# Performance work log

Hardware: AMD Instinct MI355X
Metric: run time of the kernel (lower is better)

## Reference

```python
import jax, jax.numpy as jnp
import numpy as np

N_NODES = 100000


def _segment_mean(h, src, dst, n_nodes):
    # copy_u: gather source features along edges, then mean-reduce per dst node
    msg = h[src]                                             # [E, D]
    s = jax.ops.segment_sum(msg, dst, num_segments=n_nodes)  # [N, D]
    cnt = jax.ops.segment_sum(jnp.ones((src.shape[0],), h.dtype), dst,
                              num_segments=n_nodes)          # [N]
    return s / jnp.maximum(cnt, 1.0)[:, None]


def setup_inputs() -> dict:
    key = jax.random.key(0)
    k1, k2, k3, k4, k5 = jax.random.split(key, 5)
    in_feats, n_hidden, n_classes = 128, 128, 64
    n_edges = 1600000
    features = jax.random.normal(k1, (N_NODES, in_feats), dtype=jnp.float32)
    W1 = jax.random.normal(k2, (in_feats, n_hidden), dtype=jnp.float32) * (1.0 / np.sqrt(in_feats))
    b1 = jnp.zeros((n_hidden,), jnp.float32)
    W2 = jax.random.normal(k3, (n_hidden, n_classes), dtype=jnp.float32) * (1.0 / np.sqrt(n_hidden))
    b2 = jnp.zeros((n_classes,), jnp.float32)
    src = jax.random.randint(k4, (n_edges,), 0, N_NODES, dtype=jnp.int64)
    dst = jax.random.randint(k5, (n_edges,), 0, N_NODES, dtype=jnp.int64)
    return {"features": features, "W1": W1, "b1": b1, "W2": W2, "b2": b2,
            "src": src, "dst": dst}


def reference(features, W1, b1, W2, b2, src, dst):
    # Layer 0: mean aggregation -> Linear -> relu  (dropout p=0.0 is identity)
    h = _segment_mean(features, src, dst, N_NODES)
    h = jax.nn.relu(h @ W1 + b1)
    # Layer 1: mean aggregation -> Linear (no activation on output layer)
    h = _segment_mean(h, src, dst, N_NODES)
    h = h @ W2 + b2
    return h
```

## Files before the change

kernel.cpp:

```cpp
#include <hip/hip_runtime.h>

#define N_NODES 100000
#define D 128
#define NE 1600000
#define C_OUT 64
#define NB 391
#define SENT 100000
#define P2B 256
#define P2E 6250
#define SEGSTRIDE 6400

typedef _Float16 half8 __attribute__((ext_vector_type(8)));
typedef float floatx4 __attribute__((ext_vector_type(4)));


__device__ inline half8 shfl_xor_h8(half8 v, int mask) {
    union { half8 h; int i[4]; } u;
    u.h = v;
    u.i[0] = __shfl_xor(u.i[0], mask);
    u.i[1] = __shfl_xor(u.i[1], mask);
    u.i[2] = __shfl_xor(u.i[2], mask);
    u.i[3] = __shfl_xor(u.i[3], mask);
    return u.h;
}

__device__ inline void pack_one(const float* W, _Float16* Wp, int tid, int N) {
    int l = tid & 63, p = tid >> 6;
    int nt = p >> 2, kc = p & 3;
    int quad = l >> 4, c = l & 15;
    int n = nt * 16 + c;
    half8 h;
    #pragma unroll
    for (int j = 0; j < 8; ++j) {
        int k = kc * 32 + quad * 8 + j;
        h[j] = (_Float16)W[k * N + n];
    }
    *(half8*)(Wp + (size_t)p * 512 + l * 8) = h;
}

__global__ __launch_bounds__(256) void setup_kernel(const float* __restrict__ W1,
                                                    const float* __restrict__ W2,
                                                    _Float16* __restrict__ wp1,
                                                    _Float16* __restrict__ wp2,
                                                    int* __restrict__ t1s,
                                                    int* __restrict__ t2s) {
    const int blk = blockIdx.x;
    const int t = threadIdx.x;
    if (blk < 8) {
        pack_one(W1, wp1, blk * 256 + t, 128);
    } else if (blk < 12) {
        pack_one(W2, wp2, (blk - 8) * 256 + t, 64);
    } else {
        if (t < 64) t1s[t] = 0;
        else if (t < 96) t2s[t - 64] = 0;
    }
}

__global__ __launch_bounds__(1024) void p2_part(const int* __restrict__ src,
                                                const int* __restrict__ dst,
                                                unsigned* __restrict__ gwords,
                                                int* __restrict__ ofsg) {
    __shared__ unsigned ebuf[P2E];
    __shared__ int hist[NB];
    __shared__ int ofs[NB + 1];
    __shared__ int cur[NB];
    __shared__ int wsum[8];
    const int t = threadIdx.x;
    const int base = blockIdx.x * P2E;

    for (int i = t; i < NB; i += 1024) hist[i] = 0;
    __syncthreads();

    unsigned w[7];
    int bk[7];
    #pragma unroll
    for (int r = 0; r < 7; ++r) {
        const int j = r * 1024 + t;
        if (j < P2E) {
            const int e = base + j;
            const int d = dst[e];
            w[r] = ((unsigned)(d & 255) << 20) | (unsigned)src[e];
            bk[r] = d >> 8;
            atomicAdd(&hist[bk[r]], 1);
        } else {
            bk[r] = -1;
        }
    }
    __syncthreads();

    int v = 0, incl = 0;
    if (t < 512) { v = (t < NB) ? hist[t] : 0; incl = v; }
    #pragma unroll
    for (int d = 1; d < 64; d <<= 1) {
        int y = __shfl_up(incl, d);
        if ((t & 63) >= d) incl += y;
    }
    if (t < 512 && (t & 63) == 63) wsum[t >> 6] = incl;
    __syncthreads();
    if (t < NB) {
        int ex = incl - v;
        const int wv = t >> 6;
        for (int j = 0; j < wv; ++j) ex += wsum[j];
        ofs[t] = ex;
        cur[t] = ex;
    }
    if (t == 0) ofs[NB] = P2E;
    __syncthreads();

    #pragma unroll
    for (int r = 0; r < 7; ++r) {
        if (bk[r] >= 0) {
            const int slot = atomicAdd(&cur[bk[r]], 1);
            ebuf[slot] = w[r];
        }
    }
    __syncthreads();

    unsigned* gout = gwords + (size_t)blockIdx.x * SEGSTRIDE;
    for (int i = t; i < P2E; i += 1024) gout[i] = ebuf[i];
    int* oout = ofsg + blockIdx.x * (NB + 1);
    for (int i = t; i < NB + 1; i += 1024) oout[i] = ofs[i];
}

__global__ __launch_bounds__(256) void p_sum(const int* __restrict__ ofsg,
                                             int* __restrict__ btot) {
    __shared__ int ws4[4];
    const int b = blockIdx.x;
    const int t = threadIdx.x;
    const int* row = ofsg + t * (NB + 1);
    int d = row[b + 1] - row[b];
    #pragma unroll
    for (int m = 1; m < 64; m <<= 1) d += __shfl_xor(d, m);
    if ((t & 63) == 0) ws4[t >> 6] = d;
    __syncthreads();
    if (t == 0) btot[b] = ws4[0] + ws4[1] + ws4[2] + ws4[3];
}

__global__ __launch_bounds__(512) void p_scanB(const int* __restrict__ btot,
                                               int* __restrict__ bbase) {
    __shared__ int wsum[8];
    const int t = threadIdx.x;
    int v = (t < NB) ? btot[t] : 0;
    int incl = v;
    #pragma unroll
    for (int d = 1; d < 64; d <<= 1) {
        int y = __shfl_up(incl, d);
        if ((t & 63) >= d) incl += y;
    }
    if ((t & 63) == 63) wsum[t >> 6] = incl;
    __syncthreads();
    int ex = incl - v;
    const int wv = t >> 6;
    for (int j = 0; j < wv; ++j) ex += wsum[j];
    if (t < NB) bbase[t] = ex;
    if (t == 0) bbase[NB] = NE;
}

__global__ __launch_bounds__(256) void p3_finalize(const unsigned* __restrict__ gwords,
                                                   const int* __restrict__ ofsg,
                                                   const int* __restrict__ bbase,
                                                   int* __restrict__ ptrp,
                                                   int* __restrict__ pcnt,
                                                   float* __restrict__ inv,
                                                   int* __restrict__ csr) {
    __shared__ unsigned wbuf[8192];
    __shared__ int lcnt[256];
    __shared__ int lofs[256];
    __shared__ int ws4[4];
    __shared__ int cursor;
    const int b = blockIdx.x;
    const int t = threadIdx.x;
    if (t == 0) cursor = 0;
    lcnt[t] = 0;
    __syncthreads();

    for (int blk = t; blk < P2B; blk += 256) {
        const int* row = ofsg + blk * (NB + 1);
        const int a = row[b];
        const int len = row[b + 1] - a;
        if (len > 0) {
            const int o = atomicAdd(&cursor, len);
            if (o + len <= 8192) {
                const unsigned* s = gwords + (size_t)blk * SEGSTRIDE + a;
                for (int j = 0; j < len; ++j) {
                    const unsigned w = s[j];
                    wbuf[o + j] = w;
                    atomicAdd(&lcnt[(w >> 20) & 255], 1);
                }
            }
        }
    }
    __syncthreads();

    const int tot = cursor;
    const int v = lcnt[t];
    const int pc = (v + 7) & ~7;
    int incl = pc;
    #pragma unroll
    for (int d = 1; d < 64; d <<= 1) {
        int y = __shfl_up(incl, d);
        if ((t & 63) >= d) incl += y;
    }
    if ((t & 63) == 63) ws4[t >> 6] = incl;
    __syncthreads();
    int ex = incl - pc;
    {
        const int wv = t >> 6;
        for (int j = 0; j < wv; ++j) ex += ws4[j];
    }
    const int pad_base = bbase[b] + 1792 * b;

    const int node = b * 256 + t;
    if (node < N_NODES) {
        ptrp[node] = pad_base + ex;
        pcnt[node] = pc;
        inv[node] = 1.0f / fmaxf((float)v, 1.0f);
    }
    for (int j = v; j < pc; ++j) csr[pad_base + ex + j] = SENT;

    __syncthreads();
    lofs[t] = ex;
    __syncthreads();
    for (int i = t; i < tot; i += 256) {
        const unsigned w = wbuf[i];
        const int pos = atomicAdd(&lofs[(w >> 20) & 255], 1);
        csr[pad_base + pos] = (int)(w & 0xFFFFF);
    }
}

__global__ __launch_bounds__(256) void gemm1(const float* __restrict__ A,
                                             const _Float16* __restrict__ Wp,
                                             _Float16* __restrict__ outh) {
    __shared__ __align__(16) _Float16 Wl[16384];
    __shared__ __align__(16) _Float16 Al[4096];
    const int t = threadIdx.x;
    {
        const floatx4* s4 = (const floatx4*)Wp;
        floatx4* d4 = (floatx4*)Wl;
        #pragma unroll
        for (int i = 0; i < 8; ++i) d4[t + 256 * i] = s4[t + 256 * i];
    }
    const int lane = t & 63;
    const int wave = t >> 6;
    const int row0 = blockIdx.x * 128;

    floatx4 acc[8][2];
    #pragma unroll
    for (int mt = 0; mt < 8; ++mt)
        #pragma unroll
        for (int nt = 0; nt < 2; ++nt) acc[mt][nt] = (floatx4)0.0f;

    for (int kc = 0; kc < 4; ++kc) {
        __syncthreads();
        #pragma unroll
        for (int rep = 0; rep < 2; ++rep) {
            int p = rep * 256 + t;
            int r = p >> 2, quad = p & 3;
            int row = row0 + r;
            if (row > N_NODES - 1) row = N_NODES - 1;
            const float4 x0 = *(const float4*)(A + (size_t)row * D + kc * 32 + quad * 8);
            const float4 x1 = *(const float4*)(A + (size_t)row * D + kc * 32 + quad * 8 + 4);
            half8 h;
            h[0] = (_Float16)x0.x; h[1] = (_Float16)x0.y;
            h[2] = (_Float16)x0.z; h[3] = (_Float16)x0.w;
            h[4] = (_Float16)x1.x; h[5] = (_Float16)x1.y;
            h[6] = (_Float16)x1.z; h[7] = (_Float16)x1.w;
            int mt = r >> 4, m = r & 15;
            *(half8*)(Al + mt * 512 + (quad * 16 + m) * 8) = h;
        }
        __syncthreads();
        const half8* Af = (const half8*)Al;
        const half8* Bf = (const half8*)Wl;
        half8 b0 = Bf[((wave * 2 + 0) * 4 + kc) * 64 + lane];
        half8 b1 = Bf[((wave * 2 + 1) * 4 + kc) * 64 + lane];
        #pragma unroll
        for (int mt = 0; mt < 8; ++mt) {
            half8 a = Af[mt * 64 + lane];
            acc[mt][0] = __builtin_amdgcn_mfma_f32_16x16x32_f16(a, b0, acc[mt][0], 0, 0, 0);
            acc[mt][1] = __builtin_amdgcn_mfma_f32_16x16x32_f16(a, b1, acc[mt][1], 0, 0, 0);
        }
    }

    const int quad = lane >> 4, cl = lane & 15;
    #pragma unroll
    for (int mt = 0; mt < 8; ++mt)
        #pragma unroll
        for (int nt = 0; nt < 2; ++nt) {
            int col = wave * 32 + nt * 16 + cl;
            #pragma unroll
            for (int i = 0; i < 4; ++i) {
                int row = row0 + mt * 16 + quad * 4 + i;
                if (row < N_NODES)
                    outh[(size_t)row * D + col] = (_Float16)acc[mt][nt][i];
            }
        }
}

__global__ __launch_bounds__(256) void gemm2(const _Float16* __restrict__ Ah,
                                             const _Float16* __restrict__ Wp,
                                             _Float16* __restrict__ outh) {
    __shared__ __align__(16) _Float16 Wl[8192];
    __shared__ __align__(16) _Float16 Al[4096];
    const int t = threadIdx.x;
    {
        const floatx4* s4 = (const floatx4*)Wp;
        floatx4* d4 = (floatx4*)Wl;
        #pragma unroll
        for (int i = 0; i < 4; ++i) d4[t + 256 * i] = s4[t + 256 * i];
    }
    const int lane = t & 63;
    const int wave = t >> 6;
    const int row0 = blockIdx.x * 128;

    floatx4 acc[8];
    #pragma unroll
    for (int mt = 0; mt < 8; ++mt) acc[mt] = (floatx4)0.0f;

    for (int kc = 0; kc < 4; ++kc) {
        __syncthreads();
        #pragma unroll
        for (int rep = 0; rep < 2; ++rep) {
            int p = rep * 256 + t;
            int r = p >> 2, quad = p & 3;
            int row = row0 + r;
            if (row > N_NODES - 1) row = N_NODES - 1;
            half8 h = *(const half8*)(Ah + (size_t)row * D + kc * 32 + quad * 8);
            int mt = r >> 4, m = r & 15;
            *(half8*)(Al + mt * 512 + (quad * 16 + m) * 8) = h;
        }
        __syncthreads();
        const half8* Af = (const half8*)Al;
        const half8* Bf = (const half8*)Wl;
        half8 b = Bf[(wave * 4 + kc) * 64 + lane];
        #pragma unroll
        for (int mt = 0; mt < 8; ++mt) {
            half8 a = Af[mt * 64 + lane];
            acc[mt] = __builtin_amdgcn_mfma_f32_16x16x32_f16(a, b, acc[mt], 0, 0, 0);
        }
    }

    const int quad = lane >> 4, cl = lane & 15;
    const int col = wave * 16 + cl;
    #pragma unroll
    for (int mt = 0; mt < 8; ++mt)
        #pragma unroll
        for (int i = 0; i < 4; ++i) {
            int row = row0 + mt * 16 + quad * 4 + i;
            if (row < N_NODES)
                outh[(size_t)row * C_OUT + col] = (_Float16)acc[mt][i];
        }
}

__global__ __launch_bounds__(256) void agg128h(const _Float16* __restrict__ f,
                                               const int* __restrict__ ptrp,
                                               const int* __restrict__ pcnt,
                                               const int* __restrict__ csr,
                                               const float* __restrict__ inv,
                                               const float* __restrict__ bias,
                                               _Float16* __restrict__ outh) {
    const int wave = threadIdx.x >> 6;
    const int lane = threadIdx.x & 63;
    const int q = lane & 15, hf = lane >> 4;
    const int n = blockIdx.x * 4 + wave;
    const int begin = ptrp[n];
    const int end = begin + pcnt[n];
    const float iv = inv[n];
    const half8* f8 = (const half8*)f;

    half8 acc0 = {0, 0, 0, 0, 0, 0, 0, 0};
    half8 acc1 = {0, 0, 0, 0, 0, 0, 0, 0};
    for (int base = begin; base < end; base += 64) {
        const int m = min(64, end - base);
        int edge = (lane < m) ? csr[base + lane] : SENT;
        int i = 0;
        for (; i + 16 <= m; i += 16) {
            int s0 = __shfl(edge, i + hf);
            int s1 = __shfl(edge, i + 4 + hf);
            int s2 = __shfl(edge, i + 8 + hf);
            int s3 = __shfl(edge, i + 12 + hf);
            half8 v0 = f8[(size_t)s0 * 16 + q];
            half8 v1 = f8[(size_t)s1 * 16 + q];
            half8 v2 = f8[(size_t)s2 * 16 + q];
            half8 v3 = f8[(size_t)s3 * 16 + q];
            acc0 += v0;
            acc1 += v1;
            acc0 += v2;
            acc1 += v3;
        }
        if (i < m) {
            int s0 = __shfl(edge, i + hf);
            int s1 = __shfl(edge, i + 4 + hf);
            half8 v0 = f8[(size_t)s0 * 16 + q];
            half8 v1 = f8[(size_t)s1 * 16 + q];
            acc0 += v0;
            acc1 += v1;
        }
    }
    acc0 += acc1;
    acc0 += shfl_xor_h8(acc0, 16);
    acc0 += shfl_xor_h8(acc0, 32);
    if (hf == 0) {
        const float4 b0 = ((const float4*)bias)[q * 2];
        const float4 b1 = ((const float4*)bias)[q * 2 + 1];
        half8 o;
        o[0] = (_Float16)fmaxf((float)acc0[0] * iv + b0.x, 0.f);
        o[1] = (_Float16)fmaxf((float)acc0[1] * iv + b0.y, 0.f);
        o[2] = (_Float16)fmaxf((float)acc0[2] * iv + b0.z, 0.f);
        o[3] = (_Float16)fmaxf((float)acc0[3] * iv + b0.w, 0.f);
        o[4] = (_Float16)fmaxf((float)acc0[4] * iv + b1.x, 0.f);
        o[5] = (_Float16)fmaxf((float)acc0[5] * iv + b1.y, 0.f);
        o[6] = (_Float16)fmaxf((float)acc0[6] * iv + b1.z, 0.f);
        o[7] = (_Float16)fmaxf((float)acc0[7] * iv + b1.w, 0.f);
        ((half8*)outh)[(size_t)n * 16 + q] = o;
    }
}

__global__ __launch_bounds__(256) void agg64h(const _Float16* __restrict__ f,
                                              const int* __restrict__ ptrp,
                                              const int* __restrict__ pcnt,
                                              const int* __restrict__ csr,
                                              const float* __restrict__ inv,
                                              const float* __restrict__ bias,
                                              float* __restrict__ out) {
    const int wave = threadIdx.x >> 6;
    const int lane = threadIdx.x & 63;
    const int q = lane & 7, hf = lane >> 3;
    const int n = blockIdx.x * 4 + wave;
    const int begin = ptrp[n];
    const int end = begin + pcnt[n];
    const float iv = inv[n];
    const half8* f8 = (const half8*)f;

    half8 acc0 = {0, 0, 0, 0, 0, 0, 0, 0};
    half8 acc1 = {0, 0, 0, 0, 0, 0, 0, 0};
    for (int base = begin; base < end; base += 64) {
        const int m = min(64, end - base);
        int edge = (lane < m) ? csr[base + lane] : SENT;
        int i = 0;
        for (; i + 32 <= m; i += 32) {
            int s0 = __shfl(edge, i + hf);
            int s1 = __shfl(edge, i + 8 + hf);
            int s2 = __shfl(edge, i + 16 + hf);
            int s3 = __shfl(edge, i + 24 + hf);
            half8 v0 = f8[(size_t)s0 * 8 + q];
            half8 v1 = f8[(size_t)s1 * 8 + q];
            half8 v2 = f8[(size_t)s2 * 8 + q];
            half8 v3 = f8[(size_t)s3 * 8 + q];
            acc0 += v0;
            acc1 += v1;
            acc0 += v2;
            acc1 += v3;
        }
        if (i + 16 <= m) {
            int s0 = __shfl(edge, i + hf);
            int s1 = __shfl(edge, i + 8 + hf);
            half8 v0 = f8[(size_t)s0 * 8 + q];
            half8 v1 = f8[(size_t)s1 * 8 + q];
            acc0 += v0;
            acc1 += v1;
            i += 16;
        }
        if (i < m) {
            int s = __shfl(edge, i + hf);
            acc0 += f8[(size_t)s * 8 + q];
        }
    }
    acc0 += acc1;
    acc0 += shfl_xor_h8(acc0, 8);
    acc0 += shfl_xor_h8(acc0, 16);
    acc0 += shfl_xor_h8(acc0, 32);
    if (hf == 0) {
        const float4 b0 = ((const float4*)bias)[q * 2];
        const float4 b1 = ((const float4*)bias)[q * 2 + 1];
        float4 o0, o1;
        o0.x = (float)acc0[0] * iv + b0.x;
        o0.y = (float)acc0[1] * iv + b0.y;
        o0.z = (float)acc0[2] * iv + b0.z;
        o0.w = (float)acc0[3] * iv + b0.w;
        o1.x = (float)acc0[4] * iv + b1.x;
        o1.y = (float)acc0[5] * iv + b1.y;
        o1.z = (float)acc0[6] * iv + b1.z;
        o1.w = (float)acc0[7] * iv + b1.w;
        ((float4*)out)[(size_t)n * 16 + q * 2] = o0;
        ((float4*)out)[(size_t)n * 16 + q * 2 + 1] = o1;
    }
}

extern "C" void kernel_launch(void* const* d_in, const int* in_sizes, int n_in,
                              void* d_out, int out_size, void* d_ws, size_t ws_size,
                              hipStream_t stream) {
    const float* features = (const float*)d_in[0];
    const float* W1 = (const float*)d_in[1];
    const float* b1 = (const float*)d_in[2];
    const float* W2 = (const float*)d_in[3];
    const float* b2 = (const float*)d_in[4];
    const int* src = (const int*)d_in[5];
    const int* dst = (const int*)d_in[6];
    float* out = (float*)d_out;

    char* ws = (char*)d_ws;
    int*      bbase = (int*)(ws + 0L * 4);
    int*      ofsg  = (int*)(ws + 512L * 4);
    int*      btot  = (int*)(ws + 100864L * 4);
    int*      ptrp  = (int*)(ws + 125952L * 4);
    int*      pcnt  = (int*)(ws + 225952L * 4);
    float*    inv   = (float*)(ws + 325952L * 4);
    int*      csr   = (int*)(ws + 425952L * 4);
    unsigned* gwords= (unsigned*)(ws + 2825952L * 4);
    _Float16* wp1   = (_Float16*)(ws + 4464352L * 4);
    _Float16* wp2   = (_Float16*)(ws + 4472544L * 4);
    _Float16* t1h   = (_Float16*)(ws + 4476640L * 4);
    _Float16* h1h   = (_Float16*)(ws + 10876704L * 4);
    _Float16* t2h   = (_Float16*)(ws + 17276704L * 4);

    setup_kernel<<<13, 256, 0, stream>>>(W1, W2, wp1, wp2,
                                         (int*)(t1h + (size_t)SENT * 128),
                                         (int*)(t2h + (size_t)SENT * 64));
    p2_part<<<P2B, 1024, 0, stream>>>(src, dst, gwords, ofsg);
    p_sum<<<NB, 256, 0, stream>>>(ofsg, btot);
    p_scanB<<<1, 512, 0, stream>>>(btot, bbase);
    p3_finalize<<<NB, 256, 0, stream>>>(gwords, ofsg, bbase, ptrp, pcnt, inv, csr);

    const int gemm_grid = (N_NODES + 127) / 128;

    gemm1<<<gemm_grid, 256, 0, stream>>>(features, wp1, t1h);
    agg128h<<<N_NODES / 4, 256, 0, stream>>>(t1h, ptrp, pcnt, csr, inv, b1, h1h);

    gemm2<<<gemm_grid, 256, 0, stream>>>(h1h, wp2, t2h);
    agg64h<<<N_NODES / 4, 256, 0, stream>>>(t2h, ptrp, pcnt, csr, inv, b2, out);
}
```

Before: 250.2 us.

## Fuse pipeline stages into fewer kernel launches and merge aggregation with GEMM2

Merges the weight-packing setup into the partition kernel, and the per-bucket sum into the first GEMM launch as extra blocks. The separate bucket scan is removed: each finalize block recomputes its own prefix from btot. Layer-1 aggregation is fused with the second GEMM so the aggregated hidden features stay in LDS and never go to global memory. This cuts launch count and the global round-trip of the h1 buffer. The cost is redundant prefix sums per block and heterogeneous blocks with larger shared memory that may lower occupancy.

```diff
diff --git a/kernel.cpp b/kernel.cpp
--- a/kernel.cpp
+++ b/kernel.cpp
@@ -38,28 +38,32 @@
     *(half8*)(Wp + (size_t)p * 512 + l * 8) = h;
 }
 
-__global__ __launch_bounds__(256) void setup_kernel(const float* __restrict__ W1,
+__global__ __launch_bounds__(1024) void k1_p2_setup(const int* __restrict__ src,
+                                                    const int* __restrict__ dst,
+                                                    unsigned* __restrict__ gwords,
+                                                    int* __restrict__ ofsg,
+                                                    const float* __restrict__ W1,
                                                     const float* __restrict__ W2,
                                                     _Float16* __restrict__ wp1,
                                                     _Float16* __restrict__ wp2,
                                                     int* __restrict__ t1s,
                                                     int* __restrict__ t2s) {
-    const int blk = blockIdx.x;
-    const int t = threadIdx.x;
-    if (blk < 8) {
-        pack_one(W1, wp1, blk * 256 + t, 128);
-    } else if (blk < 12) {
-        pack_one(W2, wp2, (blk - 8) * 256 + t, 64);
-    } else {
-        if (t < 64) t1s[t] = 0;
-        else if (t < 96) t2s[t - 64] = 0;
-    }
-}
-
-__global__ __launch_bounds__(1024) void p2_part(const int* __restrict__ src,
-                                                const int* __restrict__ dst,
-                                                unsigned* __restrict__ gwords,
-                                                int* __restrict__ ofsg) {
+    if (blockIdx.x >= P2B) {
+        const int blk = blockIdx.x - P2B;
+        const int t = threadIdx.x;
+        if (t < 256) {
+            if (blk < 8) {
+                pack_one(W1, wp1, blk * 256 + t, 128);
+            } else if (blk < 12) {
+                pack_one(W2, wp2, (blk - 8) * 256 + t, 64);
+            } else {
+                if (t < 64) t1s[t] = 0;
+                else if (t < 96) t2s[t - 64] = 0;
+            }
+        }
+        return;
+    }
+
     __shared__ unsigned ebuf[P2E];
     __shared__ int hist[NB];
     __shared__ int ofs[NB + 1];
@@ -122,118 +126,30 @@
     for (int i = t; i < NB + 1; i += 1024) oout[i] = ofs[i];
 }
 
-__global__ __launch_bounds__(256) void p_sum(const int* __restrict__ ofsg,
-                                             int* __restrict__ btot) {
-    __shared__ int ws4[4];
-    const int b = blockIdx.x;
+#define K2_PSUM 391
+__global__ __launch_bounds__(256) void k2_psum_gemm1(const int* __restrict__ ofsg,
+                                                     int* __restrict__ btot,
+                                                     const float* __restrict__ A,
+                                                     const _Float16* __restrict__ Wp,
+                                                     _Float16* __restrict__ outh) {
+    __shared__ __align__(16) char smem[40960];
     const int t = threadIdx.x;
-    const int* row = ofsg + t * (NB + 1);
-    int d = row[b + 1] - row[b];
-    #pragma unroll
-    for (int m = 1; m < 64; m <<= 1) d += __shfl_xor(d, m);
-    if ((t & 63) == 0) ws4[t >> 6] = d;
-    __syncthreads();
-    if (t == 0) btot[b] = ws4[0] + ws4[1] + ws4[2] + ws4[3];
-}
-
-__global__ __launch_bounds__(512) void p_scanB(const int* __restrict__ btot,
-                                               int* __restrict__ bbase) {
-    __shared__ int wsum[8];
-    const int t = threadIdx.x;
-    int v = (t < NB) ? btot[t] : 0;
-    int incl = v;
-    #pragma unroll
-    for (int d = 1; d < 64; d <<= 1) {
-        int y = __shfl_up(incl, d);
-        if ((t & 63) >= d) incl += y;
-    }
-    if ((t & 63) == 63) wsum[t >> 6] = incl;
-    __syncthreads();
-    int ex = incl - v;
-    const int wv = t >> 6;
-    for (int j = 0; j < wv; ++j) ex += wsum[j];
-    if (t < NB) bbase[t] = ex;
-    if (t == 0) bbase[NB] = NE;
-}
-
-__global__ __launch_bounds__(256) void p3_finalize(const unsigned* __restrict__ gwords,
-                                                   const int* __restrict__ ofsg,
-                                                   const int* __restrict__ bbase,
-                                                   int* __restrict__ ptrp,
-                                                   int* __restrict__ pcnt,
-                                                   float* __restrict__ inv,
-                                                   int* __restrict__ csr) {
-    __shared__ unsigned wbuf[8192];
-    __shared__ int lcnt[256];
-    __shared__ int lofs[256];
-    __shared__ int ws4[4];
-    __shared__ int cursor;
-    const int b = blockIdx.x;
-    const int t = threadIdx.x;
-    if (t == 0) cursor = 0;
-    lcnt[t] = 0;
-    __syncthreads();
-
-    for (int blk = t; blk < P2B; blk += 256) {
-        const int* row = ofsg + blk * (NB + 1);
-        const int a = row[b];
-        const int len = row[b + 1] - a;
-        if (len > 0) {
-            const int o = atomicAdd(&cursor, len);
-            if (o + len <= 8192) {
-                const unsigned* s = gwords + (size_t)blk * SEGSTRIDE + a;
-                for (int j = 0; j < len; ++j) {
-                    const unsigned w = s[j];
-                    wbuf[o + j] = w;
-                    atomicAdd(&lcnt[(w >> 20) & 255], 1);
-                }
-            }
-        }
-    }
-    __syncthreads();
-
-    const int tot = cursor;
-    const int v = lcnt[t];
-    const int pc = (v + 7) & ~7;
-    int incl = pc;
-    #pragma unroll
-    for (int d = 1; d < 64; d <<= 1) {
-        int y = __shfl_up(incl, d);
-        if ((t & 63) >= d) incl += y;
-    }
-    if ((t & 63) == 63) ws4[t >> 6] = incl;
-    __syncthreads();
-    int ex = incl - pc;
-    {
-        const int wv = t >> 6;
-        for (int j = 0; j < wv; ++j) ex += ws4[j];
-    }
-    const int pad_base = bbase[b] + 1792 * b;
-
-    const int node = b * 256 + t;
-    if (node < N_NODES) {
-        ptrp[node] = pad_base + ex;
-        pcnt[node] = pc;
-        inv[node] = 1.0f / fmaxf((float)v, 1.0f);
-    }
-    for (int j = v; j < pc; ++j) csr[pad_base + ex + j] = SENT;
-
-    __syncthreads();
-    lofs[t] = ex;
-    __syncthreads();
-    for (int i = t; i < tot; i += 256) {
-        const unsigned w = wbuf[i];
-        const int pos = atomicAdd(&lofs[(w >> 20) & 255], 1);
-        csr[pad_base + pos] = (int)(w & 0xFFFFF);
-    }
-}
-
-__global__ __launch_bounds__(256) void gemm1(const float* __restrict__ A,
-                                             const _Float16* __restrict__ Wp,
-                                             _Float16* __restrict__ outh) {
-    __shared__ __align__(16) _Float16 Wl[16384];
-    __shared__ __align__(16) _Float16 Al[4096];
-    const int t = threadIdx.x;
+
+    if (blockIdx.x < K2_PSUM) {
+        int* ws4 = (int*)smem;
+        const int b = blockIdx.x;
+        const int* row = ofsg + t * (NB + 1);
+        int d = row[b + 1] - row[b];
+        #pragma unroll
+        for (int m = 1; m < 64; m <<= 1) d += __shfl_xor(d, m);
+        if ((t & 63) == 0) ws4[t >> 6] = d;
+        __syncthreads();
+        if (t == 0) btot[b] = ws4[0] + ws4[1] + ws4[2] + ws4[3];
+        return;
+    }
+
+    _Float16* Wl = (_Float16*)smem;
+    _Float16* Al = (_Float16*)(smem + 32768);
     {
         const floatx4* s4 = (const floatx4*)Wp;
         floatx4* d4 = (floatx4*)Wl;
@@ -242,7 +158,7 @@
     }
     const int lane = t & 63;
     const int wave = t >> 6;
-    const int row0 = blockIdx.x * 128;
+    const int row0 = (blockIdx.x - K2_PSUM) * 128;
 
     floatx4 acc[8][2];
     #pragma unroll
@@ -296,11 +212,96 @@
         }
 }
 
-__global__ __launch_bounds__(256) void gemm2(const _Float16* __restrict__ Ah,
-                                             const _Float16* __restrict__ Wp,
-                                             _Float16* __restrict__ outh) {
+__global__ __launch_bounds__(256) void p3_finalize(const unsigned* __restrict__ gwords,
+                                                   const int* __restrict__ ofsg,
+                                                   const int* __restrict__ btot,
+                                                   int* __restrict__ ptrp,
+                                                   int* __restrict__ pcnt,
+                                                   float* __restrict__ inv,
+                                                   int* __restrict__ csr) {
+    __shared__ unsigned wbuf[8192];
+    __shared__ int lcnt[256];
+    __shared__ int lofs[256];
+    __shared__ int ws4[4];
+    __shared__ int cursor;
+    const int b = blockIdx.x;
+    const int t = threadIdx.x;
+    if (t == 0) cursor = 0;
+    lcnt[t] = 0;
+
+    int s = 0;
+    for (int i = t; i < b; i += 256) s += btot[i];
+    #pragma unroll
+    for (int m = 1; m < 64; m <<= 1) s += __shfl_xor(s, m);
+    if ((t & 63) == 0) ws4[t >> 6] = s;
+    __syncthreads();
+    const int bb = ws4[0] + ws4[1] + ws4[2] + ws4[3];
+    const int pad_base = bb + 1792 * b;
+
+    for (int blk = t; blk < P2B; blk += 256) {
+        const int* row = ofsg + blk * (NB + 1);
+        const int a = row[b];
+        const int len = row[b + 1] - a;
+        if (len > 0) {
+            const int o = atomicAdd(&cursor, len);
+            if (o + len <= 8192) {
+                const unsigned* sseg = gwords + (size_t)blk * SEGSTRIDE + a;
+                for (int j = 0; j < len; ++j) {
+                    const unsigned w = sseg[j];
+                    wbuf[o + j] = w;
+                    atomicAdd(&lcnt[(w >> 20) & 255], 1);
+                }
+            }
+        }
+    }
+    __syncthreads();
+
+    const int tot = cursor;
+    const int v = lcnt[t];
+    const int pc = (v + 7) & ~7;
+    int incl = pc;
+    #pragma unroll
+    for (int d = 1; d < 64; d <<= 1) {
+        int y = __shfl_up(incl, d);
+        if ((t & 63) >= d) incl += y;
+    }
+    __syncthreads();
+    if ((t & 63) == 63) ws4[t >> 6] = incl;
+    __syncthreads();
+    int ex = incl - pc;
+    {
+        const int wv = t >> 6;
+        for (int j = 0; j < wv; ++j) ex += ws4[j];
+    }
+
+    const int node = b * 256 + t;
+    if (node < N_NODES) {
+        ptrp[node] = pad_base + ex;
+        pcnt[node] = pc;
+        inv[node] = 1.0f / fmaxf((float)v, 1.0f);
+    }
+    for (int j = v; j < pc; ++j) csr[pad_base + ex + j] = SENT;
+
+    __syncthreads();
+    lofs[t] = ex;
+    __syncthreads();
+    for (int i = t; i < tot; i += 256) {
+        const unsigned w = wbuf[i];
+        const int pos = atomicAdd(&lofs[(w >> 20) & 255], 1);
+        csr[pad_base + pos] = (int)(w & 0xFFFFF);
+    }
+}
+
+__global__ __launch_bounds__(256) void k4_agg_gemm2(const _Float16* __restrict__ f,
+                                                    const int* __restrict__ ptrp,
+                                                    const int* __restrict__ pcnt,
+                                                    const int* __restrict__ csr,
+                                                    const float* __restrict__ inv,
+                                                    const float* __restrict__ bias,
+                                                    const _Float16* __restrict__ Wp,
+                                                    _Float16* __restrict__ outh) {
     __shared__ __align__(16) _Float16 Wl[8192];
-    __shared__ __align__(16) _Float16 Al[4096];
+    __shared__ __align__(16) _Float16 h1t[16 * 136];
     const int t = threadIdx.x;
     {
         const floatx4* s4 = (const floatx4*)Wp;
@@ -308,110 +309,80 @@
         #pragma unroll
         for (int i = 0; i < 4; ++i) d4[t + 256 * i] = s4[t + 256 * i];
     }
+    const int wave = t >> 6;
     const int lane = t & 63;
-    const int wave = t >> 6;
-    const int row0 = blockIdx.x * 128;
-
-    floatx4 acc[8];
-    #pragma unroll
-    for (int mt = 0; mt < 8; ++mt) acc[mt] = (floatx4)0.0f;
-
+    const int q = lane & 15, hf = lane >> 4;
+    const half8* f8 = (const half8*)f;
+
+    for (int it = 0; it < 4; ++it) {
+        const int r = wave * 4 + it;
+        const int n = blockIdx.x * 16 + r;
+        const int begin = ptrp[n];
+        const int end = begin + pcnt[n];
+        const float iv = inv[n];
+
+        half8 acc0 = {0, 0, 0, 0, 0, 0, 0, 0};
+        half8 acc1 = {0, 0, 0, 0, 0, 0, 0, 0};
+        for (int base = begin; base < end; base += 64) {
+            const int m = min(64, end - base);
+            int edge = (lane < m) ? csr[base + lane] : SENT;
+            int i = 0;
+            for (; i + 16 <= m; i += 16) {
+                int s0 = __shfl(edge, i + hf);
+                int s1 = __shfl(edge, i + 4 + hf);
+                int s2 = __shfl(edge, i + 8 + hf);
+                int s3 = __shfl(edge, i + 12 + hf);
+                half8 v0 = f8[(size_t)s0 * 16 + q];
+                half8 v1 = f8[(size_t)s1 * 16 + q];
+                half8 v2 = f8[(size_t)s2 * 16 + q];
+                half8 v3 = f8[(size_t)s3 * 16 + q];
+                acc0 += v0;
+                acc1 += v1;
+                acc0 += v2;
+                acc1 += v3;
+            }
+            if (i < m) {
+                int s0 = __shfl(edge, i + hf);
+                int s1 = __shfl(edge, i + 4 + hf);
+                half8 v0 = f8[(size_t)s0 * 16 + q];
+                half8 v1 = f8[(size_t)s1 * 16 + q];
+                acc0 += v0;
+                acc1 += v1;
+            }
+        }
+        acc0 += acc1;
+        acc0 += shfl_xor_h8(acc0, 16);
+        acc0 += shfl_xor_h8(acc0, 32);
+        if (hf == 0) {
+            const float4 b0 = ((const float4*)bias)[q * 2];
+            const float4 b1v = ((const float4*)bias)[q * 2 + 1];
+            half8 o;
+            o[0] = (_Float16)fmaxf((float)acc0[0] * iv + b0.x, 0.f);
+            o[1] = (_Float16)fmaxf((float)acc0[1] * iv + b0.y, 0.f);
+            o[2] = (_Float16)fmaxf((float)acc0[2] * iv + b0.z, 0.f);
+            o[3] = (_Float16)fmaxf((float)acc0[3] * iv + b0.w, 0.f);
+            o[4] = (_Float16)fmaxf((float)acc0[4] * iv + b1v.x, 0.f);
+            o[5] = (_Float16)fmaxf((float)acc0[5] * iv + b1v.y, 0.f);
+            o[6] = (_Float16)fmaxf((float)acc0[6] * iv + b1v.z, 0.f);
+            o[7] = (_Float16)fmaxf((float)acc0[7] * iv + b1v.w, 0.f);
+            *(half8*)(h1t + r * 136 + q * 8) = o;
+        }
+    }
+    __syncthreads();
+
+    floatx4 acc = (floatx4)0.0f;
+    #pragma unroll
     for (int kc = 0; kc < 4; ++kc) {
-        __syncthreads();
-        #pragma unroll
-        for (int rep = 0; rep < 2; ++rep) {
-            int p = rep * 256 + t;
-            int r = p >> 2, quad = p & 3;
-            int row = row0 + r;
-            if (row > N_NODES - 1) row = N_NODES - 1;
-            half8 h = *(const half8*)(Ah + (size_t)row * D + kc * 32 + quad * 8);
-            int mt = r >> 4, m = r & 15;
-            *(half8*)(Al + mt * 512 + (quad * 16 + m) * 8) = h;
-        }
-        __syncthreads();
-        const half8* Af = (const half8*)Al;
-        const half8* Bf = (const half8*)Wl;
-        half8 b = Bf[(wave * 4 + kc) * 64 + lane];
-        #pragma unroll
-        for (int mt = 0; mt < 8; ++mt) {
-            half8 a = Af[mt * 64 + lane];
-            acc[mt] = __builtin_amdgcn_mfma_f32_16x16x32_f16(a, b, acc[mt], 0, 0, 0);
-        }
-    }
-
+        half8 a = *(const half8*)(h1t + (lane & 15) * 136 + kc * 32 + (lane >> 4) * 8);
+        half8 b = ((const half8*)Wl)[(wave * 4 + kc) * 64 + lane];
+        acc = __builtin_amdgcn_mfma_f32_16x16x32_f16(a, b, acc, 0, 0, 0);
+    }
     const int quad = lane >> 4, cl = lane & 15;
     const int col = wave * 16 + cl;
     #pragma unroll
-    for (int mt = 0; mt < 8; ++mt)
-        #pragma unroll
-        for (int i = 0; i < 4; ++i) {
-            int row = row0 + mt * 16 + quad * 4 + i;
-            if (row < N_NODES)
-                outh[(size_t)row * C_OUT + col] = (_Float16)acc[mt][i];
-        }
-}
-
-__global__ __launch_bounds__(256) void agg128h(const _Float16* __restrict__ f,
-                                               const int* __restrict__ ptrp,
-                                               const int* __restrict__ pcnt,
-                                               const int* __restrict__ csr,
-                                               const float* __restrict__ inv,
-                                               const float* __restrict__ bias,
-                                               _Float16* __restrict__ outh) {
-    const int wave = threadIdx.x >> 6;
-    const int lane = threadIdx.x & 63;
-    const int q = lane & 15, hf = lane >> 4;
-    const int n = blockIdx.x * 4 + wave;
-    const int begin = ptrp[n];
-    const int end = begin + pcnt[n];
-    const float iv = inv[n];
-    const half8* f8 = (const half8*)f;
-
-    half8 acc0 = {0, 0, 0, 0, 0, 0, 0, 0};
-    half8 acc1 = {0, 0, 0, 0, 0, 0, 0, 0};
-    for (int base = begin; base < end; base += 64) {
-        const int m = min(64, end - base);
-        int edge = (lane < m) ? csr[base + lane] : SENT;
-        int i = 0;
-        for (; i + 16 <= m; i += 16) {
-            int s0 = __shfl(edge, i + hf);
-            int s1 = __shfl(edge, i + 4 + hf);
-            int s2 = __shfl(edge, i + 8 + hf);
-            int s3 = __shfl(edge, i + 12 + hf);
-            half8 v0 = f8[(size_t)s0 * 16 + q];
-            half8 v1 = f8[(size_t)s1 * 16 + q];
-            half8 v2 = f8[(size_t)s2 * 16 + q];
-            half8 v3 = f8[(size_t)s3 * 16 + q];
-            acc0 += v0;
-            acc1 += v1;
-            acc0 += v2;
-            acc1 += v3;
-        }
-        if (i < m) {
-            int s0 = __shfl(edge, i + hf);
-            int s1 = __shfl(edge, i + 4 + hf);
-            half8 v0 = f8[(size_t)s0 * 16 + q];
-            half8 v1 = f8[(size_t)s1 * 16 + q];
-            acc0 += v0;
-            acc1 += v1;
-        }
-    }
-    acc0 += acc1;
-    acc0 += shfl_xor_h8(acc0, 16);
-    acc0 += shfl_xor_h8(acc0, 32);
-    if (hf == 0) {
-        const float4 b0 = ((const float4*)bias)[q * 2];
-        const float4 b1 = ((const float4*)bias)[q * 2 + 1];
-        half8 o;
-        o[0] = (_Float16)fmaxf((float)acc0[0] * iv + b0.x, 0.f);
-        o[1] = (_Float16)fmaxf((float)acc0[1] * iv + b0.y, 0.f);
-        o[2] = (_Float16)fmaxf((float)acc0[2] * iv + b0.z, 0.f);
-        o[3] = (_Float16)fmaxf((float)acc0[3] * iv + b0.w, 0.f);
-        o[4] = (_Float16)fmaxf((float)acc0[4] * iv + b1.x, 0.f);
-        o[5] = (_Float16)fmaxf((float)acc0[5] * iv + b1.y, 0.f);
-        o[6] = (_Float16)fmaxf((float)acc0[6] * iv + b1.z, 0.f);
-        o[7] = (_Float16)fmaxf((float)acc0[7] * iv + b1.w, 0.f);
-        ((half8*)outh)[(size_t)n * 16 + q] = o;
+    for (int i = 0; i < 4; ++i) {
+        const int row = blockIdx.x * 16 + quad * 4 + i;
+        outh[(size_t)row * C_OUT + col] = (_Float16)acc[i];
     }
 }
 
@@ -499,7 +470,6 @@
     float* out = (float*)d_out;
 
     char* ws = (char*)d_ws;
-    int*      bbase = (int*)(ws + 0L * 4);
     int*      ofsg  = (int*)(ws + 512L * 4);
     int*      btot  = (int*)(ws + 100864L * 4);
     int*      ptrp  = (int*)(ws + 125952L * 4);
@@ -510,22 +480,13 @@
     _Float16* wp1   = (_Float16*)(ws + 4464352L * 4);
     _Float16* wp2   = (_Float16*)(ws + 4472544L * 4);
     _Float16* t1h   = (_Float16*)(ws + 4476640L * 4);
-    _Float16* h1h   = (_Float16*)(ws + 10876704L * 4);
     _Float16* t2h   = (_Float16*)(ws + 17276704L * 4);
 
-    setup_kernel<<<13, 256, 0, stream>>>(W1, W2, wp1, wp2,
-                                         (int*)(t1h + (size_t)SENT * 128),
-                                         (int*)(t2h + (size_t)SENT * 64));
-    p2_part<<<P2B, 1024, 0, stream>>>(src, dst, gwords, ofsg);
-    p_sum<<<NB, 256, 0, stream>>>(ofsg, btot);
-    p_scanB<<<1, 512, 0, stream>>>(btot, bbase);
-    p3_finalize<<<NB, 256, 0, stream>>>(gwords, ofsg, bbase, ptrp, pcnt, inv, csr);
-
-    const int gemm_grid = (N_NODES + 127) / 128;
-
-    gemm1<<<gemm_grid, 256, 0, stream>>>(features, wp1, t1h);
-    agg128h<<<N_NODES / 4, 256, 0, stream>>>(t1h, ptrp, pcnt, csr, inv, b1, h1h);
-
-    gemm2<<<gemm_grid, 256, 0, stream>>>(h1h, wp2, t2h);
+    k1_p2_setup<<<P2B + 13, 1024, 0, stream>>>(src, dst, gwords, ofsg, W1, W2, wp1, wp2,
+                                               (int*)(t1h + (size_t)SENT * 128),
+                                               (int*)(t2h + (size_t)SENT * 64));
+    k2_psum_gemm1<<<K2_PSUM + 782, 256, 0, stream>>>(ofsg, btot, features, wp1, t1h);
+    p3_finalize<<<NB, 256, 0, stream>>>(gwords, ofsg, btot, ptrp, pcnt, inv, csr);
+    k4_agg_gemm2<<<N_NODES / 16, 256, 0, stream>>>(t1h, ptrp, pcnt, csr, inv, b1, wp2, t2h);
     agg64h<<<N_NODES / 4, 256, 0, stream>>>(t2h, ptrp, pcnt, csr, inv, b2, out);
 }
```

After: 233.6 us. 1.07x faster.
